# Kernel tuning notes

Measured on AMD Instinct MI355X. Metric: run time of the kernel, lower is better.

The kernel has to match this reference:

```python
import jax, jax.numpy as jnp
import numpy as np

T = 8388608          # sequence length (inputs reshaped to (1, T, 1) in original)
HALF_WIDTH = 0.5     # Phi hard-codes tf.constant([[1/2.0]]) regardless of width arg


def phi(v):
    # Phi(v) = v - 0.5 if v > 0.5 ; v + 0.5 if v < -0.5 ; 0 otherwise
    return jnp.where(v > HALF_WIDTH, v - HALF_WIDTH,
                     jnp.where(v < -HALF_WIDTH, v + HALF_WIDTH, jnp.zeros_like(v)))


def setup_inputs() -> dict:
    key = jax.random.key(0)
    k1, k2 = jax.random.split(key)
    x = jax.random.normal(k1, (1, T), dtype=jnp.float32)
    # learned kernel, shape (1,1), non_neg constraint -> positive init
    weight = jax.random.uniform(k2, (1, 1), dtype=jnp.float32, minval=0.5, maxval=1.5)
    state0 = jnp.zeros((1, 1), dtype=jnp.float32)
    return {"x": x, "weight": weight, "state0": state0}


def reference(x, weight, state0):
    # scale inputs by scalar kernel, flatten to the time axis: (T,)
    xs = (x * weight[0, 0]).reshape(-1)

    def step(s, xt):
        o = phi(xt - s) + s   # hysteresis update: output is also the new state
        return o, o

    s_last, outs = jax.lax.scan(step, state0[0, 0], xs)
    outputs = outs.reshape(1, T, 1)          # matches tf.keras.backend.rnn outputs_
    final_state = s_last.reshape(1, 1)       # matches states_x[-1]
    return outputs, final_state
```

## Files before the change

kernel.cpp:

```cpp
#include <hip/hip_runtime.h>
#include <math.h>


#define T_ELEMS 8388608
#define BLOCK   256
#define EPT     32
#define EPB     (BLOCK * EPT)
#define NBLK    (T_ELEMS / EPB)

struct Op { float lo, hi; };

__device__ __forceinline__ Op combine(Op a, Op b) {
    Op r;
    r.lo = fmaxf(b.lo, fminf(b.hi, a.lo));
    r.hi = fminf(b.hi, a.hi);
    return r;
}

__device__ __forceinline__ float apply_op(Op o, float s) {
    return fmaxf(o.lo, fminf(o.hi, s));
}

__device__ __forceinline__ void fold_elem(Op& t, float e) {
    float elo = e - 0.5f, ehi = e + 0.5f;
    t.lo = fmaxf(elo, fminf(ehi, t.lo));
    t.hi = fminf(ehi, t.hi);
}

__global__ __launch_bounds__(BLOCK) void phase1(const float* __restrict__ x,
                                                const float* __restrict__ w,
                                                float2* __restrict__ blkTot) {
    __shared__ Op lds[BLOCK];
    const float wv = w[0];
    const int tid = threadIdx.x;
    const size_t base = ((size_t)blockIdx.x * BLOCK + tid) * EPT;
    const float4* xv = reinterpret_cast<const float4*>(x + base);

    Op t = { -__builtin_inff(), __builtin_inff() };
#pragma unroll
    for (int j = 0; j < EPT / 4; ++j) {
        float4 v = xv[j];
        fold_elem(t, v.x * wv);
        fold_elem(t, v.y * wv);
        fold_elem(t, v.z * wv);
        fold_elem(t, v.w * wv);
    }

    lds[tid] = t;
    __syncthreads();
#pragma unroll
    for (int off = 1; off < BLOCK; off <<= 1) {
        if ((tid & (2 * off - 1)) == 0) {
            lds[tid] = combine(lds[tid], lds[tid + off]);
        }
        __syncthreads();
    }
    if (tid == 0) {
        blkTot[blockIdx.x] = make_float2(lds[0].lo, lds[0].hi);
    }
}

__global__ __launch_bounds__(64) void phase2(const float2* __restrict__ blkTot,
                                             const float* __restrict__ state0,
                                             float* __restrict__ blkStart,
                                             float* __restrict__ finalOut) {
    const int lane = threadIdx.x;
    const int PER = NBLK / 64;
    const float s0 = state0[0];

    Op t = { -__builtin_inff(), __builtin_inff() };
    Op tots[PER];
#pragma unroll
    for (int j = 0; j < PER; ++j) {
        float2 bt = blkTot[lane * PER + j];
        Op o = { bt.x, bt.y };
        tots[j] = o;
        t = combine(t, o);
    }

    float plo = t.lo, phi_ = t.hi;
#pragma unroll
    for (int off = 1; off < 64; off <<= 1) {
        float nlo = __shfl_up(plo, off);
        float nhi = __shfl_up(phi_, off);
        if (lane >= off) {
            float newlo = fmaxf(plo, fminf(phi_, nlo));
            float newhi = fminf(phi_, nhi);
            plo = newlo; phi_ = newhi;
        }
    }
    float elo = __shfl_up(plo, 1);
    float ehi = __shfl_up(phi_, 1);
    if (lane == 0) { elo = -__builtin_inff(); ehi = __builtin_inff(); }

    float s = fmaxf(elo, fminf(ehi, s0));
#pragma unroll
    for (int j = 0; j < PER; ++j) {
        blkStart[lane * PER + j] = s;
        s = apply_op(tots[j], s);
    }
    if (lane == 63) {
        finalOut[0] = s;
    }
}

__global__ __launch_bounds__(BLOCK) void phase3(const float* __restrict__ x,
                                                const float* __restrict__ w,
                                                const float* __restrict__ blkStart,
                                                float* __restrict__ out) {
    __shared__ Op lds[BLOCK];
    const float wv = w[0];
    const int tid = threadIdx.x;
    const size_t base = ((size_t)blockIdx.x * BLOCK + tid) * EPT;
    const float4* xv = reinterpret_cast<const float4*>(x + base);

    float4 xr[EPT / 4];
    Op t = { -__builtin_inff(), __builtin_inff() };
#pragma unroll
    for (int j = 0; j < EPT / 4; ++j) {
        float4 v = xv[j];
        v.x *= wv; v.y *= wv; v.z *= wv; v.w *= wv;
        xr[j] = v;
        fold_elem(t, v.x);
        fold_elem(t, v.y);
        fold_elem(t, v.z);
        fold_elem(t, v.w);
    }

    lds[tid] = t;
    __syncthreads();
#pragma unroll
    for (int off = 1; off < BLOCK; off <<= 1) {
        Op cur = lds[tid];
        Op prev;
        bool act = (tid >= off);
        if (act) prev = lds[tid - off];
        __syncthreads();
        if (act) cur = combine(prev, cur);
        lds[tid] = cur;
        __syncthreads();
    }

    Op excl;
    if (tid == 0) {
        excl.lo = -__builtin_inff(); excl.hi = __builtin_inff();
    } else {
        excl = lds[tid - 1];
    }

    float s = blkStart[blockIdx.x];
    s = apply_op(excl, s);

    float4* ov = reinterpret_cast<float4*>(out + base);
#pragma unroll
    for (int j = 0; j < EPT / 4; ++j) {
        float4 v = xr[j];
        float4 o;
        s = fmaxf(v.x - 0.5f, fminf(v.x + 0.5f, s)); o.x = s;
        s = fmaxf(v.y - 0.5f, fminf(v.y + 0.5f, s)); o.y = s;
        s = fmaxf(v.z - 0.5f, fminf(v.z + 0.5f, s)); o.z = s;
        s = fmaxf(v.w - 0.5f, fminf(v.w + 0.5f, s)); o.w = s;
        ov[j] = o;
    }
}

extern "C" void kernel_launch(void* const* d_in, const int* in_sizes, int n_in,
                              void* d_out, int out_size, void* d_ws, size_t ws_size,
                              hipStream_t stream) {
    const float* x  = (const float*)d_in[0];
    const float* w  = (const float*)d_in[1];
    const float* s0 = (const float*)d_in[2];
    float* out = (float*)d_out;

    float2* blkTot   = (float2*)d_ws;
    float*  blkStart = (float*)((char*)d_ws + NBLK * sizeof(float2));

    phase1<<<NBLK, BLOCK, 0, stream>>>(x, w, blkTot);
    phase2<<<1, 64, 0, stream>>>(blkTot, s0, blkStart, out + T_ELEMS);
    phase3<<<NBLK, BLOCK, 0, stream>>>(x, w, blkStart, out);
}
```

Measured before the change: 102.9 us.

## Shrink per-thread work to one float4 and use wave-shuffle block scans

Each thread now handles 4 elements instead of 32, which gives eight times as many blocks. The LDS tree reduction and Hillis-Steele scan are replaced by wavefront shuffle scans with a small LDS combine across waves. Phase2 moves to 256 threads to handle the larger block-total array and re-reads the totals instead of keeping them in registers. The aim is to raise memory-level parallelism and cut LDS barriers. The cost is more blocks, more block-level scan overhead per element, and a larger serial phase2 workload.

```diff
diff --git a/kernel.cpp b/kernel.cpp
--- a/kernel.cpp
+++ b/kernel.cpp
@@ -4,9 +4,14 @@
 
 #define T_ELEMS 8388608
 #define BLOCK   256
-#define EPT     32
+#define EPT     4
 #define EPB     (BLOCK * EPT)
 #define NBLK    (T_ELEMS / EPB)
+#define P2T     256
+#define P2PER   (NBLK / P2T)
+
+#define NEG_INF (-__builtin_inff())
+#define POS_INF (__builtin_inff())
 
 struct Op { float lo, hi; };
 
@@ -27,141 +32,122 @@
     t.hi = fminf(ehi, t.hi);
 }
 
+__device__ __forceinline__ Op thread_op(float4 v) {
+    Op t = { v.x - 0.5f, v.x + 0.5f };
+    fold_elem(t, v.y);
+    fold_elem(t, v.z);
+    fold_elem(t, v.w);
+    return t;
+}
+
+__device__ __forceinline__ Op wave_incl_scan(Op t, int lane) {
+#pragma unroll
+    for (int off = 1; off < 64; off <<= 1) {
+        float nlo = __shfl_up(t.lo, off);
+        float nhi = __shfl_up(t.hi, off);
+        if (lane >= off) {
+            Op prev = { nlo, nhi };
+            t = combine(prev, t);
+        }
+    }
+    return t;
+}
+
+__device__ __forceinline__ Op block_excl_from_incl(Op incl, int lane, int wid, Op* lds_wt) {
+    if (lane == 63) lds_wt[wid] = incl;
+    __syncthreads();
+    Op wpre = { NEG_INF, POS_INF };
+    for (int k = 0; k < wid; ++k) wpre = combine(wpre, lds_wt[k]);
+    float elo = __shfl_up(incl.lo, 1);
+    float ehi = __shfl_up(incl.hi, 1);
+    Op excl;
+    if (lane == 0) { excl.lo = NEG_INF; excl.hi = POS_INF; }
+    else           { excl.lo = elo;     excl.hi = ehi;     }
+    return combine(wpre, excl);
+}
+
 __global__ __launch_bounds__(BLOCK) void phase1(const float* __restrict__ x,
                                                 const float* __restrict__ w,
                                                 float2* __restrict__ blkTot) {
-    __shared__ Op lds[BLOCK];
+    __shared__ Op wt[BLOCK / 64];
     const float wv = w[0];
     const int tid = threadIdx.x;
-    const size_t base = ((size_t)blockIdx.x * BLOCK + tid) * EPT;
-    const float4* xv = reinterpret_cast<const float4*>(x + base);
+    const size_t base = (size_t)blockIdx.x * EPB + (size_t)tid * EPT;
+    float4 v = *reinterpret_cast<const float4*>(x + base);
+    v.x *= wv; v.y *= wv; v.z *= wv; v.w *= wv;
+    Op t = thread_op(v);
 
-    Op t = { -__builtin_inff(), __builtin_inff() };
 #pragma unroll
-    for (int j = 0; j < EPT / 4; ++j) {
-        float4 v = xv[j];
-        fold_elem(t, v.x * wv);
-        fold_elem(t, v.y * wv);
-        fold_elem(t, v.z * wv);
-        fold_elem(t, v.w * wv);
+    for (int off = 1; off < 64; off <<= 1) {
+        float nlo = __shfl_down(t.lo, off);
+        float nhi = __shfl_down(t.hi, off);
+        Op nb = { nlo, nhi };
+        t = combine(t, nb);
     }
-
-    lds[tid] = t;
+    if ((tid & 63) == 0) wt[tid >> 6] = t;
     __syncthreads();
+    if (tid == 0) {
+        Op b = wt[0];
 #pragma unroll
-    for (int off = 1; off < BLOCK; off <<= 1) {
-        if ((tid & (2 * off - 1)) == 0) {
-            lds[tid] = combine(lds[tid], lds[tid + off]);
-        }
-        __syncthreads();
-    }
-    if (tid == 0) {
-        blkTot[blockIdx.x] = make_float2(lds[0].lo, lds[0].hi);
+        for (int k = 1; k < BLOCK / 64; ++k) b = combine(b, wt[k]);
+        blkTot[blockIdx.x] = make_float2(b.lo, b.hi);
     }
 }
 
-__global__ __launch_bounds__(64) void phase2(const float2* __restrict__ blkTot,
-                                             const float* __restrict__ state0,
-                                             float* __restrict__ blkStart,
-                                             float* __restrict__ finalOut) {
-    const int lane = threadIdx.x;
-    const int PER = NBLK / 64;
-    const float s0 = state0[0];
+__global__ __launch_bounds__(P2T) void phase2(const float2* __restrict__ blkTot,
+                                              const float* __restrict__ state0,
+                                              float* __restrict__ blkStart,
+                                              float* __restrict__ finalOut) {
+    __shared__ Op wt[P2T / 64];
+    const int tid = threadIdx.x;
+    const int lane = tid & 63, wid = tid >> 6;
 
-    Op t = { -__builtin_inff(), __builtin_inff() };
-    Op tots[PER];
-#pragma unroll
-    for (int j = 0; j < PER; ++j) {
-        float2 bt = blkTot[lane * PER + j];
-        Op o = { bt.x, bt.y };
-        tots[j] = o;
+    Op t = { NEG_INF, POS_INF };
+#pragma unroll 4
+    for (int j = 0; j < P2PER; ++j) {
+        float2 b = blkTot[tid * P2PER + j];
+        Op o = { b.x, b.y };
         t = combine(t, o);
     }
 
-    float plo = t.lo, phi_ = t.hi;
-#pragma unroll
-    for (int off = 1; off < 64; off <<= 1) {
-        float nlo = __shfl_up(plo, off);
-        float nhi = __shfl_up(phi_, off);
-        if (lane >= off) {
-            float newlo = fmaxf(plo, fminf(phi_, nlo));
-            float newhi = fminf(phi_, nhi);
-            plo = newlo; phi_ = newhi;
-        }
+    Op incl = wave_incl_scan(t, lane);
+    Op myex = block_excl_from_incl(incl, lane, wid, wt);
+
+    float s = apply_op(myex, state0[0]);
+#pragma unroll 4
+    for (int j = 0; j < P2PER; ++j) {
+        blkStart[tid * P2PER + j] = s;
+        float2 b = blkTot[tid * P2PER + j];
+        Op o = { b.x, b.y };
+        s = apply_op(o, s);
     }
-    float elo = __shfl_up(plo, 1);
-    float ehi = __shfl_up(phi_, 1);
-    if (lane == 0) { elo = -__builtin_inff(); ehi = __builtin_inff(); }
-
-    float s = fmaxf(elo, fminf(ehi, s0));
-#pragma unroll
-    for (int j = 0; j < PER; ++j) {
-        blkStart[lane * PER + j] = s;
-        s = apply_op(tots[j], s);
-    }
-    if (lane == 63) {
-        finalOut[0] = s;
-    }
+    if (tid == P2T - 1) finalOut[0] = s;
 }
 
 __global__ __launch_bounds__(BLOCK) void phase3(const float* __restrict__ x,
                                                 const float* __restrict__ w,
                                                 const float* __restrict__ blkStart,
                                                 float* __restrict__ out) {
-    __shared__ Op lds[BLOCK];
+    __shared__ Op wt[BLOCK / 64];
     const float wv = w[0];
     const int tid = threadIdx.x;
-    const size_t base = ((size_t)blockIdx.x * BLOCK + tid) * EPT;
-    const float4* xv = reinterpret_cast<const float4*>(x + base);
+    const int lane = tid & 63, wid = tid >> 6;
+    const size_t base = (size_t)blockIdx.x * EPB + (size_t)tid * EPT;
+    float4 v = *reinterpret_cast<const float4*>(x + base);
+    v.x *= wv; v.y *= wv; v.z *= wv; v.w *= wv;
 
-    float4 xr[EPT / 4];
-    Op t = { -__builtin_inff(), __builtin_inff() };
-#pragma unroll
-    for (int j = 0; j < EPT / 4; ++j) {
-        float4 v = xv[j];
-        v.x *= wv; v.y *= wv; v.z *= wv; v.w *= wv;
-        xr[j] = v;
-        fold_elem(t, v.x);
-        fold_elem(t, v.y);
-        fold_elem(t, v.z);
-        fold_elem(t, v.w);
-    }
+    Op t = thread_op(v);
+    Op incl = wave_incl_scan(t, lane);
+    Op myex = block_excl_from_incl(incl, lane, wid, wt);
 
-    lds[tid] = t;
-    __syncthreads();
-#pragma unroll
-    for (int off = 1; off < BLOCK; off <<= 1) {
-        Op cur = lds[tid];
-        Op prev;
-        bool act = (tid >= off);
-        if (act) prev = lds[tid - off];
-        __syncthreads();
-        if (act) cur = combine(prev, cur);
-        lds[tid] = cur;
-        __syncthreads();
-    }
+    float s = apply_op(myex, blkStart[blockIdx.x]);
 
-    Op excl;
-    if (tid == 0) {
-        excl.lo = -__builtin_inff(); excl.hi = __builtin_inff();
-    } else {
-        excl = lds[tid - 1];
-    }
-
-    float s = blkStart[blockIdx.x];
-    s = apply_op(excl, s);
-
-    float4* ov = reinterpret_cast<float4*>(out + base);
-#pragma unroll
-    for (int j = 0; j < EPT / 4; ++j) {
-        float4 v = xr[j];
-        float4 o;
-        s = fmaxf(v.x - 0.5f, fminf(v.x + 0.5f, s)); o.x = s;
-        s = fmaxf(v.y - 0.5f, fminf(v.y + 0.5f, s)); o.y = s;
-        s = fmaxf(v.z - 0.5f, fminf(v.z + 0.5f, s)); o.z = s;
-        s = fmaxf(v.w - 0.5f, fminf(v.w + 0.5f, s)); o.w = s;
-        ov[j] = o;
-    }
+    float4 o;
+    s = fmaxf(v.x - 0.5f, fminf(v.x + 0.5f, s)); o.x = s;
+    s = fmaxf(v.y - 0.5f, fminf(v.y + 0.5f, s)); o.y = s;
+    s = fmaxf(v.z - 0.5f, fminf(v.z + 0.5f, s)); o.z = s;
+    s = fmaxf(v.w - 0.5f, fminf(v.w + 0.5f, s)); o.w = s;
+    *reinterpret_cast<float4*>(out + base) = o;
 }
 
 extern "C" void kernel_launch(void* const* d_in, const int* in_sizes, int n_in,
@@ -176,6 +162,6 @@
     float*  blkStart = (float*)((char*)d_ws + NBLK * sizeof(float2));
 
     phase1<<<NBLK, BLOCK, 0, stream>>>(x, w, blkTot);
-    phase2<<<1, 64, 0, stream>>>(blkTot, s0, blkStart, out + T_ELEMS);
+    phase2<<<1, P2T, 0, stream>>>(blkTot, s0, blkStart, out + T_ELEMS);
     phase3<<<NBLK, BLOCK, 0, stream>>>(x, w, blkStart, out);
 }
```

New measurement: 102.6 us. About the same (-0.3%).
